# Performance work log

Hardware: AMD Instinct MI355X
Metric: run time of the kernel (lower is better)

## Reference

```python
import jax, jax.numpy as jnp
import numpy as np

B, N, C = 8, 1025, 768
NUM_HEADS = 12
HEAD_DIM = C // NUM_HEADS  # 64, also depthwise-conv channel count
HW = (32, 32)              # N = 1 + 32*32 (cls token)
SCALE = HEAD_DIM ** -0.5
VALUE_MASK_FILL = -10000.0
LN_EPS = 1e-5


def setup_inputs() -> dict:
    key = jax.random.key(0)
    ks = jax.random.split(key, 12)
    s = 0.02
    inp = {
        "x": jax.random.normal(ks[0], (B, N, C), jnp.float32),
        "mask": jax.random.bernoulli(ks[1], 0.9, (B, N)),
        "Wq": jax.random.normal(ks[2], (C, C), jnp.float32) * s,
        "Wk": jax.random.normal(ks[3], (C, C), jnp.float32) * s,
        "Wv": jax.random.normal(ks[4], (C, C), jnp.float32) * s,
        "pool_q_w": jax.random.normal(ks[5], (HEAD_DIM, 1, 3, 3), jnp.float32) * s,
        "pool_k_w": jax.random.normal(ks[6], (HEAD_DIM, 1, 3, 3), jnp.float32) * s,
        "pool_v_w": jax.random.normal(ks[7], (HEAD_DIM, 1, 3, 3), jnp.float32) * s,
        "gq": jnp.ones((HEAD_DIM,), jnp.float32),
        "bq": jnp.zeros((HEAD_DIM,), jnp.float32),
        "gk": jnp.ones((HEAD_DIM,), jnp.float32),
        "bk": jnp.zeros((HEAD_DIM,), jnp.float32),
        "gv": jnp.ones((HEAD_DIM,), jnp.float32),
        "bv": jnp.zeros((HEAD_DIM,), jnp.float32),
        "Wp": jax.random.normal(ks[8], (C, C), jnp.float32) * s,
        "bp": jnp.zeros((C,), jnp.float32),
    }
    return inp


def _layernorm(t, g, b):
    m = jnp.mean(t, axis=-1, keepdims=True)
    v = jnp.var(t, axis=-1, keepdims=True)
    return (t - m) * jax.lax.rsqrt(v + LN_EPS) * g + b


def _depthwise(t, w):
    # t: [BH, D, H, W], w: [D, 1, 3, 3] depthwise, stride 1, SAME padding
    return jax.lax.conv_general_dilated(
        t, w, window_strides=(1, 1), padding="SAME",
        dimension_numbers=("NCHW", "OIHW", "NCHW"),
        feature_group_count=t.shape[1])


def _attn_pool(t, w, g, b):
    # t: [B, H, N, D] with leading cls token; pool spatial tokens, norm after
    Bb, Hh, Nn, D = t.shape
    cls_tok, spat = t[:, :, :1], t[:, :, 1:]
    Hs, Ws = HW
    spat = spat.reshape(Bb * Hh, Hs, Ws, D).transpose(0, 3, 1, 2)
    spat = _depthwise(spat, w)
    spat = spat.reshape(Bb, Hh, D, Hs * Ws).transpose(0, 1, 3, 2)
    t = jnp.concatenate([cls_tok, spat], axis=2)
    return _layernorm(t, g, b)


def reference(x, mask, Wq, Wk, Wv, pool_q_w, pool_k_w, pool_v_w,
              gq, bq, gk, bk, gv, bv, Wp, bp):
    Bb, Nn, Cc = x.shape
    # QKV projections (no bias), split heads -> [B, H, N, D]
    q = (x @ Wq.T).reshape(Bb, Nn, NUM_HEADS, HEAD_DIM).transpose(0, 2, 1, 3)
    k = (x @ Wk.T).reshape(Bb, Nn, NUM_HEADS, HEAD_DIM).transpose(0, 2, 1, 3)
    v = (x @ Wv.T).reshape(Bb, Nn, NUM_HEADS, HEAD_DIM).transpose(0, 2, 1, 3)
    q = _attn_pool(q, pool_q_w, gq, bq)
    k = _attn_pool(k, pool_k_w, gk, bk)
    v = _attn_pool(v, pool_v_w, gv, bv)
    attn = jnp.einsum("bhqd,bhkd->bhqk", q, k) * SCALE
    # mask: [B, N] bool; broadcast as (B,1,N,1), False -> value_mask_fill
    attn = jnp.where(mask[:, None, :, None], attn, VALUE_MASK_FILL)
    attn = jax.nn.softmax(attn, axis=-1)
    attn_origin = attn
    out = jnp.einsum("bhqk,bhkd->bhqd", attn, v)
    # residual pooling, skipping the cls token
    out = jnp.concatenate([out[:, :, :1], out[:, :, 1:] + q[:, :, 1:]], axis=2)
    out = out.transpose(0, 2, 1, 3).reshape(Bb, Nn, Cc)
    out = out @ Wp.T + bp
    return out, attn_origin
```

## Files before the change

kernel.cpp:

```cpp
#include <hip/hip_runtime.h>
#include <hip/hip_bf16.h>
#include <cstdint>
#include <cstddef>

typedef unsigned short u16;
typedef __attribute__((ext_vector_type(8))) short bf16x8;
typedef __attribute__((ext_vector_type(4))) float f32x4;

#define MFMA16(a,b,c) __builtin_amdgcn_mfma_f32_16x16x32_bf16(a,b,c,0,0,0)
#define GLL16(gp, lp) __builtin_amdgcn_global_load_lds( \
    (const __attribute__((address_space(1))) void*)(gp), \
    (__attribute__((address_space(3))) void*)(lp), 16, 0, 0)

static constexpr int kB = 8, kH = 12, kN = 1025, kC = 768, kD = 64;
static constexpr int kBH = kB*kH;
static constexpr int kNP = 1056;
static constexpr int kM  = kB*kN;
static constexpr float kScale = 0.125f;

__device__ __forceinline__ u16 f2b(float f){
  unsigned u = __builtin_bit_cast(unsigned, f);
  u = (u + 0x7fffu + ((u>>16)&1u)) >> 16;
  return (u16)u;
}
__device__ __forceinline__ float b2f(u16 s){
  unsigned u = ((unsigned)s)<<16;
  return __builtin_bit_cast(float, u);
}

__global__ __launch_bounds__(256) void k_prep(const float4* __restrict__ x,
    const float* __restrict__ w0, const float* __restrict__ w1,
    const float* __restrict__ w2, const float* __restrict__ w3,
    const unsigned char* __restrict__ m,
    u16* __restrict__ xb, u16* __restrict__ wb, int* __restrict__ maskn){
  __shared__ int cnt;
  const int bid = blockIdx.x;
  if (bid < 6150){
    int i = bid*256 + threadIdx.x;
    float4 v = x[i];
    ushort4 o; o.x=f2b(v.x); o.y=f2b(v.y); o.z=f2b(v.z); o.w=f2b(v.w);
    *reinterpret_cast<ushort4*>(xb + (size_t)i*4) = o;
  } else if (bid < 8454){
    int j = (bid-6150)*256 + threadIdx.x;
    int sel = j/147456, i = j - sel*147456;
    const float* ws[4] = {w0,w1,w2,w3};
    float4 v = reinterpret_cast<const float4*>(ws[sel])[i];
    ushort4 o; o.x=f2b(v.x); o.y=f2b(v.y); o.z=f2b(v.z); o.w=f2b(v.w);
    *reinterpret_cast<ushort4*>(wb + (size_t)sel*589824 + (size_t)i*4) = o;
  } else {
    if (threadIdx.x==0) cnt = 0;
    __syncthreads();
    int local = 0;
    for (int i=threadIdx.x; i<1024; i+=256) local += (m[i]!=0);
    atomicAdd(&cnt, local);
    __syncthreads();
    bool b8 = (cnt > 512);
    int lb = bid - 8454;
    for (int i = lb*256 + threadIdx.x; i < kM; i += 32*256){
      int v = b8 ? (m[i]!=0) : (reinterpret_cast<const int*>(m)[i] != 0);
      maskn[i] = v;
    }
  }
}

template<int MODE>
__global__ __launch_bounds__(256) void k_gemm128(const u16* __restrict__ A,
      const u16* __restrict__ wb, const float* __restrict__ bias,
      u16* __restrict__ outb, float* __restrict__ outf){
  __shared__ union SM {
    struct { u16 a[128*32]; u16 b[128*32]; } s;
    u16 c[128*136];
  } sm;
  const int m0 = blockIdx.x*128;
  const int N0 = blockIdx.y*128;
  const int sel = (MODE==0) ? (N0/768) : 3;
  const int jb  = (MODE==0) ? (N0%768) : N0;
  const u16* W = wb + (size_t)sel*589824;
  const int t = threadIdx.x;
  const int wave = t>>6, lane = t&63;
  const int g = lane>>4, cl = lane&15;
  const int wr2 = (wave>>1)*64, wc2 = (wave&1)*64;

  const int cid0 = wave*64 + lane;
  const int cid1 = cid0 + 256;
  const int ar0 = m0 + (cid0>>2) < kM ? m0 + (cid0>>2) : kM-1;
  const int ar1 = m0 + (cid1>>2) < kM ? m0 + (cid1>>2) : kM-1;
  const int ac0 = (cid0&3)<<3, ac1 = (cid1&3)<<3;
  const int br0 = jb + (cid0>>2), br1 = jb + (cid1>>2);
  u16* lA0 = &sm.s.a[(wave*64)*8];
  u16* lA1 = &sm.s.a[(256 + wave*64)*8];
  u16* lB0 = &sm.s.b[(wave*64)*8];
  u16* lB1 = &sm.s.b[(256 + wave*64)*8];

  f32x4 acc[4][4];
  #pragma unroll
  for (int i=0;i<4;i++)
    #pragma unroll
    for (int j=0;j<4;j++) acc[i][j] = (f32x4){0.f,0.f,0.f,0.f};

  for (int k0=0; k0<768; k0+=32){
    __syncthreads();
    GLL16(A + (size_t)ar0*768 + k0 + ac0, lA0);
    GLL16(A + (size_t)ar1*768 + k0 + ac1, lA1);
    GLL16(W + (size_t)br0*768 + k0 + ac0, lB0);
    GLL16(W + (size_t)br1*768 + k0 + ac1, lB1);
    __syncthreads();
    bf16x8 af[4], bfg[4];
    #pragma unroll
    for (int fm=0; fm<4; fm++)
      af[fm] = *reinterpret_cast<const bf16x8*>(&sm.s.a[(wr2+fm*16+cl)*32 + g*8]);
    #pragma unroll
    for (int fn=0; fn<4; fn++)
      bfg[fn] = *reinterpret_cast<const bf16x8*>(&sm.s.b[(wc2+fn*16+cl)*32 + g*8]);
    #pragma unroll
    for (int fm=0; fm<4; fm++)
      #pragma unroll
      for (int fn=0; fn<4; fn++)
        acc[fm][fn] = MFMA16(af[fm], bfg[fn], acc[fm][fn]);
  }

  if (MODE==0){
    __syncthreads();
    #pragma unroll
    for (int fm=0; fm<4; fm++)
      #pragma unroll
      for (int fn=0; fn<4; fn++)
        #pragma unroll
        for (int i=0;i<4;i++){
          int r = wr2 + fm*16 + g*4 + i;
          int c = wc2 + fn*16 + cl;
          sm.c[r*136 + c] = f2b(acc[fm][fn][i]);
        }
    __syncthreads();
    #pragma unroll
    for (int it=0; it<8; it++){
      int cid = t + it*256;
      int r = cid >> 4, cc = (cid & 15) * 8;
      int gm = m0 + r;
      if (gm < kM){
        *reinterpret_cast<uint4*>(&outb[(size_t)gm*2304 + N0 + cc]) =
            *reinterpret_cast<const uint4*>(&sm.c[r*136 + cc]);
      }
    }
  } else {
    #pragma unroll
    for (int fm=0; fm<4; fm++)
      #pragma unroll
      for (int fn=0; fn<4; fn++)
        #pragma unroll
        for (int i=0;i<4;i++){
          int gm = m0 + wr2 + fm*16 + g*4 + i;
          if (gm >= kM) continue;
          int gc = jb + wc2 + fn*16 + cl;
          outf[(size_t)gm*768 + gc] = acc[fm][fn][i] + bias[gc];
        }
  }
}

__global__ __launch_bounds__(256) void k_pool3(const u16* __restrict__ qkvmat,
    const float* __restrict__ wq, const float* __restrict__ wk, const float* __restrict__ wv,
    const float* __restrict__ gq, const float* __restrict__ bq,
    const float* __restrict__ gk, const float* __restrict__ bk,
    const float* __restrict__ gv, const float* __restrict__ bv,
    u16* __restrict__ Qp, u16* __restrict__ Kp, u16* __restrict__ Vt){
  __shared__ u16 vt[64][72];
  const int which = blockIdx.y;
  const float* w9 = (which==0)?wq:(which==1)?wk:wv;
  const float* gg = (which==0)?gq:(which==1)?gk:gv;
  const float* bb2= (which==0)?bq:(which==1)?bk:bv;
  u16* out = (which==0)?Qp:(which==1)?Kp:Vt;

  const int wave = threadIdx.x>>6, d = threadIdx.x&63;
  const int nb  = blockIdx.x % 17;
  const int bh  = blockIdx.x / 17;
  const int b = bh/12, h = bh - b*12;
  const int np0 = nb*64;
  const u16* base = qkvmat + ((size_t)b*1025)*2304 + which*768 + h*64;

  float wreg[9];
  #pragma unroll
  for (int j=0;j<9;j++) wreg[j] = w9[d*9+j];
  const float gd = gg[d], bd = bb2[d];

  for (int iter=0; iter<16; ++iter){
    const int np = np0 + iter*4 + wave;
    float v = 0.f;
    if (np < kN){
      if (np == 0){
        v = b2f(base[d]);
      } else {
        int y = (np-1)>>5, x = (np-1)&31;
        #pragma unroll
        for (int ky=0; ky<3; ky++){
          int yy = y+ky-1;
          if (yy<0 || yy>31) continue;
          #pragma unroll
          for (int kx=0; kx<3; kx++){
            int xx = x+kx-1;
            if (xx<0 || xx>31) continue;
            v += wreg[ky*3+kx] * b2f(base[(size_t)(1+yy*32+xx)*2304 + d]);
          }
        }
      }
      float s = v, s2 = v*v;
      #pragma unroll
      for (int off=1; off<64; off<<=1){ s += __shfl_xor(s, off); s2 += __shfl_xor(s2, off); }
      float mean = s*(1.f/64.f);
      float var  = s2*(1.f/64.f) - mean*mean;
      v = (v-mean)*rsqrtf(var+1e-5f)*gd + bd;
    }
    if (which==2) vt[d][iter*4+wave] = f2b(v);
    else if (np < kNP) out[((size_t)bh*kNP + np)*kD + d] = f2b(v);
  }

  if (which==2){
    __syncthreads();
    const int dr = threadIdx.x>>2, seg = threadIdx.x&3;
    if (np0 + seg*16 < kNP){
      u16* dst = Vt + ((size_t)bh*kD + dr)*kNP + np0 + seg*16;
      *reinterpret_cast<uint4*>(dst)     = *reinterpret_cast<const uint4*>(&vt[dr][seg*16]);
      *reinterpret_cast<uint4*>(dst + 8) = *reinterpret_cast<const uint4*>(&vt[dr][seg*16+8]);
    }
  }
}

__global__ __launch_bounds__(256) void k_attn(const u16* __restrict__ Qp, const u16* __restrict__ Kp,
    const u16* __restrict__ Vt, const int* __restrict__ maskn,
    float* __restrict__ attn_out, u16* __restrict__ ctx){
  constexpr int LDE = 1064;
  __shared__ u16 E[16*LDE];
  __shared__ float Lrow[16];
  __shared__ float Linv[16];
  const int wave = threadIdx.x>>6, lane = threadIdx.x&63;
  const int xcd  = blockIdx.x & 7;
  const int slot = blockIdx.x >> 3;
  const int bh = xcd*12 + slot/65;
  const int qt = slot%65;
  const int b  = bh / 12, h = bh - b*12;
  const int qbase = qt*16;
  const int g = lane>>4, cl = lane&15;

  if (threadIdx.x < 16) Lrow[threadIdx.x] = 0.f;
  __syncthreads();

  const u16* qrow = Qp + ((size_t)bh*kNP + (qbase + cl))*kD + g*8;
  bf16x8 aq0 = *reinterpret_cast<const bf16x8*>(qrow);
  bf16x8 aq1 = *reinterpret_cast<const bf16x8*>(qrow + 32);

  float mq[4];
  #pragma unroll
  for (int i=0;i<4;i++){
    int qi = qbase + g*4 + i;
    mq[i] = (qi<kN && maskn[b*kN+qi]!=0) ? kScale : 0.f;
  }

  const u16* kb = Kp + (size_t)bh*kNP*kD;
  float rsum[4] = {0.f,0.f,0.f,0.f};
  #pragma unroll 2
  for (int kt=wave; kt<33; kt+=4){
    const int ktb = kt*32;
    const u16* kr = kb + (size_t)(ktb+cl)*kD + g*8;
    bf16x8 b00 = *reinterpret_cast<const bf16x8*>(kr);
    bf16x8 b01 = *reinterpret_cast<const bf16x8*>(kr+32);
    bf16x8 b10 = *reinterpret_cast<const bf16x8*>(kr+1024);
    bf16x8 b11 = *reinterpret_cast<const bf16x8*>(kr+1024+32);
    f32x4 s0 = {0.f,0.f,0.f,0.f}, s1 = {0.f,0.f,0.f,0.f};
    s0 = MFMA16(aq0,b00,s0); s0 = MFMA16(aq1,b01,s0);
    s1 = MFMA16(aq0,b10,s1); s1 = MFMA16(aq1,b11,s1);
    const bool v0 = (ktb+cl)<kN, v1 = (ktb+16+cl)<kN;
    #pragma unroll
    for (int i=0;i<4;i++){
      int row = g*4+i;
      float e0 = v0 ? __expf(s0[i]*mq[i]) : 0.f;
      float e1 = v1 ? __expf(s1[i]*mq[i]) : 0.f;
      rsum[i] += e0 + e1;
      E[row*LDE + ktb + cl]      = f2b(e0);
      E[row*LDE + ktb + 16 + cl] = f2b(e1);
    }
  }
  #pragma unroll
  for (int off=1; off<16; off<<=1){
    #pragma unroll
    for (int i=0;i<4;i++) rsum[i] += __shfl_xor(rsum[i], off);
  }
  if (cl == 0){
    #pragma unroll
    for (int i=0;i<4;i++) atomicAdd(&Lrow[g*4+i], rsum[i]);
  }
  __syncthreads();
  if (threadIdx.x < 16) Linv[threadIdx.x] = 1.f/Lrow[threadIdx.x];
  __syncthreads();

  {
    size_t S = (size_t)bh*kN*kN + (size_t)qbase*kN;
    float* tp = attn_out + S;
    int rows = kN - qbase; if (rows > 16) rows = 16;
    int T = rows*kN;
    int head = (int)((4 - (S & 3)) & 3);
    int body4 = (T - head) >> 2;
    int tail = T - head - body4*4;
    int t = threadIdx.x;
    if (t < head){
      int e = t;
      unsigned row = ((unsigned)(e*16369))>>24;
      int col = e - (int)row*kN;
      tp[e] = b2f(E[row*LDE+col]) * Linv[row];
    }
    if (t < tail){
      int e = head + body4*4 + t;
      unsigned row = ((unsigned)(e*16369))>>24;
      int col = e - (int)row*kN;
      tp[e] = b2f(E[row*LDE+col]) * Linv[row];
    }
    for (int idx = t; idx < body4; idx += 256){
      int e = head + idx*4;
      unsigned row0 = ((unsigned)(e*16369))>>24;
      unsigned row3 = ((unsigned)((e+3)*16369))>>24;
      float4 vv;
      if (row0 == row3){
        int col = e - (int)row0*kN;
        const u16* ep = &E[row0*LDE + col];
        float li = Linv[row0];
        vv.x = b2f(ep[0])*li; vv.y = b2f(ep[1])*li;
        vv.z = b2f(ep[2])*li; vv.w = b2f(ep[3])*li;
      } else {
        float tmp[4];
        #pragma unroll
        for (int j=0;j<4;j++){
          int ee = e+j;
          unsigned row = ((unsigned)(ee*16369))>>24;
          int col = ee - (int)row*kN;
          tmp[j] = b2f(E[row*LDE+col]) * Linv[row];
        }
        vv.x=tmp[0]; vv.y=tmp[1]; vv.z=tmp[2]; vv.w=tmp[3];
      }
      *reinterpret_cast<float4*>(tp + e) = vv;
    }
  }

  const int d0 = wave*16;
  f32x4 oacc = (f32x4){0.f,0.f,0.f,0.f};
  const u16* vb = Vt + ((size_t)bh*kD + d0 + cl)*kNP;
  for (int kt0=0; kt0<32; kt0+=4){
    bf16x8 pa[4], vv[4];
    #pragma unroll
    for (int j=0;j<4;j++){
      const int ko = (kt0+j)*32 + g*8;
      pa[j] = *reinterpret_cast<const bf16x8*>(&E[cl*LDE + ko]);
      vv[j] = *reinterpret_cast<const bf16x8*>(vb + ko);
    }
    #pragma unroll
    for (int j=0;j<4;j++) oacc = MFMA16(pa[j], vv[j], oacc);
  }
  {
    const int ko = 32*32 + g*8;
    bf16x8 pa = *reinterpret_cast<const bf16x8*>(&E[cl*LDE + ko]);
    bf16x8 vv = *reinterpret_cast<const bf16x8*>(vb + ko);
    oacc = MFMA16(pa, vv, oacc);
  }
  #pragma unroll
  for (int i=0;i<4;i++){
    int row = g*4+i, qi = qbase+row;
    if (qi < kN){
      float val = oacc[i] * Linv[row];
      int dd = d0 + cl;
      if (qi >= 1) val += b2f(Qp[((size_t)bh*kNP + qi)*kD + dd]);
      ctx[((size_t)(b*kN + qi))*kC + h*kD + dd] = f2b(val);
    }
  }
}

extern "C" void kernel_launch(void* const* d_in, const int* in_sizes, int n_in,
                              void* d_out, int out_size, void* d_ws, size_t ws_size,
                              hipStream_t stream) {
  const float* x    = (const float*)d_in[0];
  const void*  msk  = d_in[1];
  const float* Wq   = (const float*)d_in[2];
  const float* Wk   = (const float*)d_in[3];
  const float* Wv   = (const float*)d_in[4];
  const float* pw_q = (const float*)d_in[5];
  const float* pw_k = (const float*)d_in[6];
  const float* pw_v = (const float*)d_in[7];
  const float* gq   = (const float*)d_in[8];
  const float* bq   = (const float*)d_in[9];
  const float* gk   = (const float*)d_in[10];
  const float* bk   = (const float*)d_in[11];
  const float* gv   = (const float*)d_in[12];
  const float* bv   = (const float*)d_in[13];
  const float* Wp   = (const float*)d_in[14];
  const float* bp   = (const float*)d_in[15];

  char* ws = (char*)d_ws;
  u16* xb     = (u16*)(ws + 0);
  u16* wb     = (u16*)(ws + 12595200);
  int* maskn  = (int*)(ws + 17313792);
  u16* qkvmat = (u16*)(ws + 17346816);
  u16* Qp     = (u16*)(ws + 55132416);
  u16* Kp     = (u16*)(ws + 68108544);
  u16* Vt     = (u16*)(ws + 81084672);
  u16* ctx    = (u16*)(ws + 17346816);

  float* out1 = (float*)d_out;
  float* attn = out1 + (size_t)kM*kC;

  k_prep<<<8486, 256, 0, stream>>>(reinterpret_cast<const float4*>(x),
                                   Wq, Wk, Wv, Wp, (const unsigned char*)msk,
                                   xb, wb, maskn);
  k_gemm128<0><<<dim3(65,18), 256, 0, stream>>>(xb, wb, nullptr, qkvmat, nullptr);
  k_pool3<<<dim3(96*17,3), 256, 0, stream>>>(qkvmat, pw_q, pw_k, pw_v,
                                             gq, bq, gk, bk, gv, bv, Qp, Kp, Vt);
  k_attn<<<96*65, 256, 0, stream>>>(Qp, Kp, Vt, maskn, attn, ctx);
  k_gemm128<1><<<dim3(65,6), 256, 0, stream>>>(ctx, wb, bp, nullptr, out1);
}
```

Baseline: 434.5 us.

## Add XCD-aware block swizzle, halve GEMM epilogue LDS, raise MFMA priority

Block indices in both GEMMs and the pooling kernel are remapped so that consecutive logical tiles land on the same XCD, which should improve L2 reuse of shared rows and columns. The QKV GEMM epilogue now stages output in two 64-row phases, shrinking the shared-memory union to allow more resident blocks, at the cost of extra barriers. The attention kernel wraps its MFMA sequences in s_setprio so matrix work is issued ahead of other waves.

```diff
diff --git a/kernel.cpp b/kernel.cpp
--- a/kernel.cpp
+++ b/kernel.cpp
@@ -26,6 +26,11 @@
 __device__ __forceinline__ float b2f(u16 s){
   unsigned u = ((unsigned)s)<<16;
   return __builtin_bit_cast(float, u);
+}
+__device__ __forceinline__ int xcd_swz(int orig, int nwg){
+  int q = nwg>>3, r = nwg&7;
+  int xcd = orig&7, idx = orig>>3;
+  return (xcd<r ? xcd*(q+1) : r*(q+1)+(xcd-r)*q) + idx;
 }
 
 __global__ __launch_bounds__(256) void k_prep(const float4* __restrict__ x,
@@ -69,10 +74,11 @@
       u16* __restrict__ outb, float* __restrict__ outf){
   __shared__ union SM {
     struct { u16 a[128*32]; u16 b[128*32]; } s;
-    u16 c[128*136];
+    u16 c2[64*136];
   } sm;
-  const int m0 = blockIdx.x*128;
-  const int N0 = blockIdx.y*128;
+  const int wg = xcd_swz(blockIdx.x, gridDim.x);
+  const int m0 = (wg % 65)*128;
+  const int N0 = (wg / 65)*128;
   const int sel = (MODE==0) ? (N0/768) : 3;
   const int jb  = (MODE==0) ? (N0%768) : N0;
   const u16* W = wb + (size_t)sel*589824;
@@ -120,26 +126,31 @@
   }
 
   if (MODE==0){
-    __syncthreads();
-    #pragma unroll
-    for (int fm=0; fm<4; fm++)
+    #pragma unroll
+    for (int ph=0; ph<2; ++ph){
+      __syncthreads();
+      if ((wave>>1) == ph){
+        #pragma unroll
+        for (int fm=0; fm<4; fm++)
+          #pragma unroll
+          for (int fn=0; fn<4; fn++)
+            #pragma unroll
+            for (int i=0;i<4;i++){
+              int r = fm*16 + g*4 + i;
+              int c = wc2 + fn*16 + cl;
+              sm.c2[r*136 + c] = f2b(acc[fm][fn][i]);
+            }
+      }
+      __syncthreads();
       #pragma unroll
-      for (int fn=0; fn<4; fn++)
-        #pragma unroll
-        for (int i=0;i<4;i++){
-          int r = wr2 + fm*16 + g*4 + i;
-          int c = wc2 + fn*16 + cl;
-          sm.c[r*136 + c] = f2b(acc[fm][fn][i]);
+      for (int it=0; it<4; it++){
+        int cid = t + it*256;
+        int r = cid >> 4, cc = (cid & 15) * 8;
+        int gm = m0 + ph*64 + r;
+        if (gm < kM){
+          *reinterpret_cast<uint4*>(&outb[(size_t)gm*2304 + N0 + cc]) =
+              *reinterpret_cast<const uint4*>(&sm.c2[r*136 + cc]);
         }
-    __syncthreads();
-    #pragma unroll
-    for (int it=0; it<8; it++){
-      int cid = t + it*256;
-      int r = cid >> 4, cc = (cid & 15) * 8;
-      int gm = m0 + r;
-      if (gm < kM){
-        *reinterpret_cast<uint4*>(&outb[(size_t)gm*2304 + N0 + cc]) =
-            *reinterpret_cast<const uint4*>(&sm.c[r*136 + cc]);
       }
     }
   } else {
@@ -171,8 +182,9 @@
   u16* out = (which==0)?Qp:(which==1)?Kp:Vt;
 
   const int wave = threadIdx.x>>6, d = threadIdx.x&63;
-  const int nb  = blockIdx.x % 17;
-  const int bh  = blockIdx.x / 17;
+  const int wg  = xcd_swz(blockIdx.x, 96*17);
+  const int nb  = wg % 17;
+  const int bh  = wg / 17;
   const int b = bh/12, h = bh - b*12;
   const int np0 = nb*64;
   const u16* base = qkvmat + ((size_t)b*1025)*2304 + which*768 + h*64;
@@ -265,8 +277,10 @@
     bf16x8 b10 = *reinterpret_cast<const bf16x8*>(kr+1024);
     bf16x8 b11 = *reinterpret_cast<const bf16x8*>(kr+1024+32);
     f32x4 s0 = {0.f,0.f,0.f,0.f}, s1 = {0.f,0.f,0.f,0.f};
+    __builtin_amdgcn_s_setprio(1);
     s0 = MFMA16(aq0,b00,s0); s0 = MFMA16(aq1,b01,s0);
     s1 = MFMA16(aq0,b10,s1); s1 = MFMA16(aq1,b11,s1);
+    __builtin_amdgcn_s_setprio(0);
     const bool v0 = (ktb+cl)<kN, v1 = (ktb+16+cl)<kN;
     #pragma unroll
     for (int i=0;i<4;i++){
@@ -349,8 +363,10 @@
       pa[j] = *reinterpret_cast<const bf16x8*>(&E[cl*LDE + ko]);
       vv[j] = *reinterpret_cast<const bf16x8*>(vb + ko);
     }
+    __builtin_amdgcn_s_setprio(1);
     #pragma unroll
     for (int j=0;j<4;j++) oacc = MFMA16(pa[j], vv[j], oacc);
+    __builtin_amdgcn_s_setprio(0);
   }
   {
     const int ko = 32*32 + g*8;
@@ -406,9 +422,9 @@
   k_prep<<<8486, 256, 0, stream>>>(reinterpret_cast<const float4*>(x),
                                    Wq, Wk, Wv, Wp, (const unsigned char*)msk,
                                    xb, wb, maskn);
-  k_gemm128<0><<<dim3(65,18), 256, 0, stream>>>(xb, wb, nullptr, qkvmat, nullptr);
+  k_gemm128<0><<<65*18, 256, 0, stream>>>(xb, wb, nullptr, qkvmat, nullptr);
   k_pool3<<<dim3(96*17,3), 256, 0, stream>>>(qkvmat, pw_q, pw_k, pw_v,
                                              gq, bq, gk, bk, gv, bv, Qp, Kp, Vt);
   k_attn<<<96*65, 256, 0, stream>>>(Qp, Kp, Vt, maskn, attn, ctx);
-  k_gemm128<1><<<dim3(65,6), 256, 0, stream>>>(ctx, wb, bp, nullptr, out1);
-}
+  k_gemm128<1><<<65*6, 256, 0, stream>>>(ctx, wb, bp, nullptr, out1);
+}
```

After: 412.3 us. 5.1% less time.
